# Performance work log

Hardware: AMD Instinct MI355X
Metric: run time of the kernel (lower is better)

The kernel has to match this reference:

```python
import jax, jax.numpy as jnp
import numpy as np

N_NODES = 100000
N_RADIAL = 16  # columns 0..15
N_CONICAL = 16  # columns 16..31


def setup_inputs() -> dict:
    key = jax.random.key(0)
    k1, k2, k3, k4 = jax.random.split(key, 4)
    x = jax.random.normal(k1, (N_NODES, 32), dtype=jnp.float32)
    edge_index = jax.random.randint(k2, (2, 1600000), 0, N_NODES, dtype=jnp.int32)
    W1 = jax.random.normal(k3, (32, 128), dtype=jnp.float32) * 0.1
    b1 = jnp.zeros((128,), dtype=jnp.float32)
    W2 = jax.random.normal(k4, (128, 32), dtype=jnp.float32) * 0.1
    b2 = jnp.zeros((32,), dtype=jnp.float32)
    return {"x": x, "edge_index": edge_index, "W1": W1, "b1": b1, "W2": W2, "b2": b2}


def reference(x, edge_index, W1, b1, W2, b2):
    # slice radial / conical feature channels
    radial = x[:, :N_RADIAL]            # [N, 16]
    conical = x[:, N_RADIAL:N_RADIAL + N_CONICAL]  # [N, 16]

    i, j = edge_index[0], edge_index[1]
    rows = jnp.concatenate([i, j])      # symmetrized COO rows [2E]
    cols = jnp.concatenate([j, i])      # symmetrized COO cols [2E]

    # coalesce()+sparse.mm == segment-sum over all (duplicated) entries
    neighbor_sum = jax.ops.segment_sum(conical[cols], rows, num_segments=N_NODES)  # [N, 16]
    deg = jax.ops.segment_sum(jnp.ones_like(rows, dtype=x.dtype), rows, num_segments=N_NODES)
    deg = jnp.clip(deg, 1.0)[:, None]   # bincount(...).clamp(min=1)
    agg = neighbor_sum / deg            # mean aggregation

    combined = jnp.concatenate([radial, agg], axis=1)  # [N, 32]
    h = jax.nn.relu(combined @ W1 + b1)
    out = h @ W2 + b2                   # [N, 32]
    return out
```

## Files before the change

kernel.cpp:

```cpp
#include <hip/hip_runtime.h>
#include <hip/hip_fp16.h>

#define N_NODES  100000
#define N_RADIAL 16
#define N_CONICAL 16

#define NPB    256
#define NBKT   ((N_NODES + NPB - 1) / NPB)
#define NBLK_A 256
#define BTHR   512
#define CHUNK  12500
#define BINSTRIDE 12544
#define CAP    10240

__global__ __launch_bounds__(BTHR) void binfuse_kernel(
    const int* __restrict__ idx, const float* __restrict__ x,
    __half2* __restrict__ xcon2,
    const float* __restrict__ W1, const float* __restrict__ W2,
    float* __restrict__ W1t, float* __restrict__ W2t,
    unsigned int* __restrict__ binned, int* __restrict__ cnts,
    int* __restrict__ offs, int total, int E) {
    int b = blockIdx.x, tid = threadIdx.x;
    if (b >= NBLK_A) {
        int pb = b - NBLK_A;
        if (pb == 0) {
            for (int i = tid; i < 4096; i += BTHR) {
                int c = i >> 7, k = i & 127;
                W1t[k * 32 + c] = W1[i];
                int kk = i >> 5, o = i & 31;
                W2t[o * 128 + kk] = W2[i];
            }
        } else {
            int t = (pb - 1) * BTHR + tid;
            if (t < N_NODES * 4) {
                int n = t >> 2, p = t & 3;
                float4 v = *((const float4*)(x + (size_t)n * 32 + 16) + p);
                __half2 h0 = __floats2half2_rn(v.x, v.y);
                __half2 h1 = __floats2half2_rn(v.z, v.w);
                uint2 st;
                st.x = *(unsigned int*)&h0; st.y = *(unsigned int*)&h1;
                *(uint2*)(xcon2 + 2 * t) = st;
            }
        }
        return;
    }

    __shared__ int cnt[NBKT];
    __shared__ int loff[NBKT];
    __shared__ unsigned int stage[CHUNK];
    for (int i = tid; i < NBKT; i += BTHR) cnt[i] = 0;
    __syncthreads();

    int lo = b * CHUNK;
    int cofs = (lo >= E) ? -E : E;
    const int4* rp = (const int4*)(idx + lo);
    const int4* cp = (const int4*)(idx + lo + cofs);
    int nq = CHUNK >> 2;

    #pragma unroll 1
    for (int q = tid; q < nq; q += BTHR) {
        int4 r = rp[q];
        atomicAdd(&cnt[r.x >> 8], 1);
        atomicAdd(&cnt[r.y >> 8], 1);
        atomicAdd(&cnt[r.z >> 8], 1);
        atomicAdd(&cnt[r.w >> 8], 1);
    }
    __syncthreads();

    if (tid < 64) {
        int c[7]; int s = 0;
        #pragma unroll
        for (int u = 0; u < 7; u++) {
            int i = tid * 7 + u;
            c[u] = (i < NBKT) ? cnt[i] : 0;
            s += c[u];
        }
        int t = s;
        #pragma unroll
        for (int off = 1; off < 64; off <<= 1) {
            int u = __shfl_up(t, off, 64);
            if (tid >= off) t += u;
        }
        int ex = t - s;
        #pragma unroll
        for (int u = 0; u < 7; u++) {
            int i = tid * 7 + u;
            if (i < NBKT) { loff[i] = ex; ex += c[u]; }
        }
    }
    __syncthreads();

    for (int i = tid; i < NBKT; i += BTHR) {
        cnts[i * NBLK_A + b] = cnt[i];
        offs[i * NBLK_A + b] = loff[i];
    }
    __syncthreads();

    #pragma unroll 1
    for (int q = tid; q < nq; q += BTHR) {
        int4 r = rp[q];
        int4 c = cp[q];
        int p0 = atomicAdd(&loff[r.x >> 8], 1);
        int p1 = atomicAdd(&loff[r.y >> 8], 1);
        int p2 = atomicAdd(&loff[r.z >> 8], 1);
        int p3 = atomicAdd(&loff[r.w >> 8], 1);
        stage[p0] = ((unsigned int)(r.x & 255) << 17) | (unsigned int)c.x;
        stage[p1] = ((unsigned int)(r.y & 255) << 17) | (unsigned int)c.y;
        stage[p2] = ((unsigned int)(r.z & 255) << 17) | (unsigned int)c.z;
        stage[p3] = ((unsigned int)(r.w & 255) << 17) | (unsigned int)c.w;
    }
    __syncthreads();

    unsigned int* dst = binned + (size_t)b * BINSTRIDE;
    for (int i = tid; i < CHUNK; i += BTHR) dst[i] = stage[i];
}

__global__ __launch_bounds__(1024, 2) void agg_kernel(
    const __half* __restrict__ xcon, const int* __restrict__ cnts,
    const int* __restrict__ offs,
    const unsigned int* __restrict__ binned, __half* __restrict__ agg) {
    __shared__ unsigned int sedge[CAP];
    __shared__ int scnt[NPB];
    __shared__ int soff[NPB];
    int b = blockIdx.x, tid = threadIdx.x;
    if (tid < NPB) scnt[tid] = 0;
    __syncthreads();

    int sub = tid >> 2, l = tid & 3;
    int sc  = cnts[b * NBLK_A + sub];
    unsigned int base = (unsigned int)sub * BINSTRIDE
                      + (unsigned int)offs[b * NBLK_A + sub];

    for (int j = l; j < sc; j += 4)
        atomicAdd(&scnt[binned[base + j] >> 17], 1);
    __syncthreads();

    if (tid < 64) {
        int i0 = tid * 4;
        int c0 = scnt[i0], c1 = scnt[i0 + 1], c2 = scnt[i0 + 2], c3 = scnt[i0 + 3];
        int s = c0 + c1 + c2 + c3;
        int t = s;
        #pragma unroll
        for (int off = 1; off < 64; off <<= 1) {
            int u = __shfl_up(t, off, 64);
            if (tid >= off) t += u;
        }
        int ex = t - s;
        soff[i0]     = ex;
        soff[i0 + 1] = ex + c0;
        soff[i0 + 2] = ex + c0 + c1;
        soff[i0 + 3] = ex + c0 + c1 + c2;
    }
    __syncthreads();

    for (int j = l; j < sc; j += 4) {
        unsigned int p = binned[base + j];
        int pos = atomicAdd(&soff[p >> 17], 1);
        sedge[pos] = p & 0x1FFFFu;
    }
    __syncthreads();

    if (tid < 2 * NPB) {
        int nl = tid >> 1, q = tid & 1;
        int c  = scnt[nl];
        int s0 = soff[nl] - c;
        float a0 = 0.f, a1 = 0.f, a2 = 0.f, a3 = 0.f;
        float a4 = 0.f, a5 = 0.f, a6 = 0.f, a7 = 0.f;
        #pragma unroll 2
        for (int k = 0; k < c; k++) {
            int col = (int)sedge[s0 + k];
            uint4 raw = ((const uint4*)(xcon + (size_t)col * 16))[q];
            float2 f0 = __half22float2(*(const __half2*)&raw.x);
            float2 f1 = __half22float2(*(const __half2*)&raw.y);
            float2 f2 = __half22float2(*(const __half2*)&raw.z);
            float2 f3 = __half22float2(*(const __half2*)&raw.w);
            a0 += f0.x; a1 += f0.y; a2 += f1.x; a3 += f1.y;
            a4 += f2.x; a5 += f2.y; a6 += f3.x; a7 += f3.y;
        }
        int n = b * NPB + nl;
        if (n < N_NODES) {
            float inv = 1.0f / (float)max(c, 1);
            __half2 h0 = __floats2half2_rn(a0 * inv, a1 * inv);
            __half2 h1 = __floats2half2_rn(a2 * inv, a3 * inv);
            __half2 h2 = __floats2half2_rn(a4 * inv, a5 * inv);
            __half2 h3 = __floats2half2_rn(a6 * inv, a7 * inv);
            uint4 st;
            st.x = *(unsigned int*)&h0; st.y = *(unsigned int*)&h1;
            st.z = *(unsigned int*)&h2; st.w = *(unsigned int*)&h3;
            *(uint4*)(agg + (size_t)n * 16 + q * 8) = st;
        }
    }
}

__global__ __launch_bounds__(512, 4) void mlp_kernel(
    const float* __restrict__ x, const __half* __restrict__ agg,
    const float* __restrict__ W1t, const float* __restrict__ b1,
    const float* __restrict__ W2t, const float* __restrict__ b2,
    float* __restrict__ out, int N) {
    __shared__ __half2 H2[64 * 64];
    int tid  = threadIdx.x;
    int lane = tid & 63;
    int ws   = __builtin_amdgcn_readfirstlane(tid >> 6);
    int n    = blockIdx.x * 64 + lane;
    int nc   = min(n, N - 1);

    float comb[32];
    const float4* xr = (const float4*)(x + (size_t)nc * 32);
    #pragma unroll
    for (int c = 0; c < 4; c++) {
        float4 v = xr[c];
        comb[c*4+0] = v.x; comb[c*4+1] = v.y;
        comb[c*4+2] = v.z; comb[c*4+3] = v.w;
    }
    const __half2* ar = (const __half2*)(agg + (size_t)nc * 16);
    #pragma unroll
    for (int c = 0; c < 8; c++) {
        float2 f = __half22float2(ar[c]);
        comb[16 + 2*c]     = f.x;
        comb[16 + 2*c + 1] = f.y;
    }

    #pragma unroll
    for (int i = 0; i < 16; i += 2) {
        int k0 = ws * 16 + i;
        const float* w1a = W1t + k0 * 32;
        const float* w1b = w1a + 32;
        float ha = b1[k0], hb = b1[k0 + 1];
        #pragma unroll
        for (int c = 0; c < 32; c++) {
            ha = fmaf(comb[c], w1a[c], ha);
            hb = fmaf(comb[c], w1b[c], hb);
        }
        ha = fmaxf(ha, 0.f); hb = fmaxf(hb, 0.f);
        H2[(k0 >> 1) * 64 + lane] = __floats2half2_rn(ha, hb);
    }
    __syncthreads();

    int o0 = ws * 4;
    const float* w20 = W2t + (o0 + 0) * 128;
    const float* w21 = W2t + (o0 + 1) * 128;
    const float* w22 = W2t + (o0 + 2) * 128;
    const float* w23 = W2t + (o0 + 3) * 128;
    float acc0 = b2[o0+0], acc1 = b2[o0+1], acc2 = b2[o0+2], acc3 = b2[o0+3];
    #pragma unroll 8
    for (int kp = 0; kp < 64; kp++) {
        float2 h = __half22float2(H2[kp * 64 + lane]);
        int k0 = 2 * kp;
        acc0 = fmaf(h.x, w20[k0], acc0); acc0 = fmaf(h.y, w20[k0+1], acc0);
        acc1 = fmaf(h.x, w21[k0], acc1); acc1 = fmaf(h.y, w21[k0+1], acc1);
        acc2 = fmaf(h.x, w22[k0], acc2); acc2 = fmaf(h.y, w22[k0+1], acc2);
        acc3 = fmaf(h.x, w23[k0], acc3); acc3 = fmaf(h.y, w23[k0+1], acc3);
    }
    if (n < N) {
        float* op = out + (size_t)n * 32 + o0;
        op[0] = acc0; op[1] = acc1; op[2] = acc2; op[3] = acc3;
    }
}

extern "C" void kernel_launch(void* const* d_in, const int* in_sizes, int n_in,
                              void* d_out, int out_size, void* d_ws, size_t ws_size,
                              hipStream_t stream) {
    const float* x   = (const float*)d_in[0];
    const int*   idx = (const int*)d_in[1];
    const float* W1  = (const float*)d_in[2];
    const float* b1  = (const float*)d_in[3];
    const float* W2  = (const float*)d_in[4];
    const float* b2  = (const float*)d_in[5];
    float* out = (float*)d_out;

    const int E = in_sizes[1] / 2;
    const int total = 2 * E;

    char* base = (char*)d_ws;
    __half*       agg    = (__half*)base;
    __half*       xcon   = (__half*)(base + 3203072);
    float*        W1t    = (float*)(base + 6406144);
    float*        W2t    = (float*)(base + 6422528);
    int*          cnts   = (int*)(base + 6438912);
    int*          offs   = (int*)(base + 6839296);
    unsigned int* binned = (unsigned int*)(base + 7239680);

    int pack_blocks = (N_NODES * 4 + BTHR - 1) / BTHR;
    binfuse_kernel<<<NBLK_A + 1 + pack_blocks, BTHR, 0, stream>>>(
        idx, x, (__half2*)xcon, W1, W2, W1t, W2t,
        binned, cnts, offs, total, E);
    agg_kernel<<<NBKT, 1024, 0, stream>>>(xcon, cnts, offs, binned, agg);
    mlp_kernel<<<(N_NODES + 63) / 64, 512, 0, stream>>>(
        x, agg, W1t, b1, W2t, b2, out, N_NODES);
}
```

Before: 151.6 us.

## Double binning blocks, cache bucket entries in registers, remap blocks across XCDs

The binning stage now uses 500 blocks with smaller chunks, so more blocks take part in the scatter. In the aggregation kernel each sub-bin is read by 2 threads instead of 4, and the first 24 entries per thread are held in registers across both counting passes instead of being read from global memory twice. Block IDs are also remapped so that buckets next to each other land on the same XCD, which should improve L2 locality. The cost is more register pressure and more per-bucket count/offset metadata to read.

```diff
diff --git a/kernel.cpp b/kernel.cpp
--- a/kernel.cpp
+++ b/kernel.cpp
@@ -7,10 +7,10 @@
 
 #define NPB    256
 #define NBKT   ((N_NODES + NPB - 1) / NPB)
-#define NBLK_A 256
+#define NBLK_A 500
 #define BTHR   512
-#define CHUNK  12500
-#define BINSTRIDE 12544
+#define CHUNK  6400
+#define BINSTRIDE 6400
 #define CAP    10240
 
 __global__ __launch_bounds__(BTHR) void binfuse_kernel(
@@ -122,16 +122,34 @@
     __shared__ unsigned int sedge[CAP];
     __shared__ int scnt[NPB];
     __shared__ int soff[NPB];
-    int b = blockIdx.x, tid = threadIdx.x;
+    int orig = blockIdx.x;
+    int xcd = orig & 7, i8 = orig >> 3;
+    const int qq = NBKT >> 3, rr = NBKT & 7;
+    int b = (xcd < rr) ? xcd * (qq + 1) + i8
+                       : rr * (qq + 1) + (xcd - rr) * qq + i8;
+    int tid = threadIdx.x;
     if (tid < NPB) scnt[tid] = 0;
     __syncthreads();
 
-    int sub = tid >> 2, l = tid & 3;
-    int sc  = cnts[b * NBLK_A + sub];
-    unsigned int base = (unsigned int)sub * BINSTRIDE
-                      + (unsigned int)offs[b * NBLK_A + sub];
-
-    for (int j = l; j < sc; j += 4)
+    int sub = tid >> 1, l = tid & 1;
+    int sc = 0; unsigned int base = 0;
+    if (sub < NBLK_A) {
+        sc   = cnts[b * NBLK_A + sub];
+        base = (unsigned int)sub * BINSTRIDE
+             + (unsigned int)offs[b * NBLK_A + sub];
+    }
+
+    unsigned int ev[12];
+    #pragma unroll
+    for (int u = 0; u < 12; u++) {
+        int j = l + 2 * u;
+        ev[u] = 0u;
+        if (j < sc) {
+            ev[u] = binned[base + j];
+            atomicAdd(&scnt[ev[u] >> 17], 1);
+        }
+    }
+    for (int j = l + 24; j < sc; j += 2)
         atomicAdd(&scnt[binned[base + j] >> 17], 1);
     __syncthreads();
 
@@ -153,7 +171,16 @@
     }
     __syncthreads();
 
-    for (int j = l; j < sc; j += 4) {
+    #pragma unroll
+    for (int u = 0; u < 12; u++) {
+        int j = l + 2 * u;
+        if (j < sc) {
+            unsigned int p = ev[u];
+            int pos = atomicAdd(&soff[p >> 17], 1);
+            sedge[pos] = p & 0x1FFFFu;
+        }
+    }
+    for (int j = l + 24; j < sc; j += 2) {
         unsigned int p = binned[base + j];
         int pos = atomicAdd(&soff[p >> 17], 1);
         sedge[pos] = p & 0x1FFFFu;
@@ -277,8 +304,8 @@
     float*        W1t    = (float*)(base + 6406144);
     float*        W2t    = (float*)(base + 6422528);
     int*          cnts   = (int*)(base + 6438912);
-    int*          offs   = (int*)(base + 6839296);
-    unsigned int* binned = (unsigned int*)(base + 7239680);
+    int*          offs   = (int*)(base + 7241728);
+    unsigned int* binned = (unsigned int*)(base + 8044544);
 
     int pack_blocks = (N_NODES * 4 + BTHR - 1) / BTHR;
     binfuse_kernel<<<NBLK_A + 1 + pack_blocks, BTHR, 0, stream>>>(
```

Measured after the change: 149.2 us. Within noise of the previous version (-1.5%).
